# Performance work log

Hardware: AMD Instinct MI355X
Metric: run time of the kernel (lower is better)

The kernel has to match this reference:

```python
import jax, jax.numpy as jnp
import numpy as np

N_C, N_F = 25000, 100000   # coarse / fine node counts
E_C, E_F = 100000, 400000  # coarse / fine edge counts
W, F_IN, F_OUT = 128, 128, 4


def _fnn2(x, w1, b1, w2, b2):
    # 2-layer FNN (fnns_depth=2) with SELU, dropout=0 (eval)
    return jax.nn.selu(x @ w1 + b1) @ w2 + b2


def _interaction(v, e, src, dst, n, ew1, eb1, ew2, eb2, nw1, nb1, nw2, nb2):
    # InteractionNetwork: edge update (gather) -> mean scatter -> node update, residuals
    e = _fnn2(jnp.concatenate([e, v[src], v[dst]], axis=-1), ew1, eb1, ew2, eb2) + e
    s = jax.ops.segment_sum(e, dst, num_segments=n)
    cnt = jax.ops.segment_sum(jnp.ones((e.shape[0], 1), e.dtype), dst, num_segments=n)
    agg = s / jnp.maximum(cnt, 1.0)  # 'mean' aggregation
    v = _fnn2(jnp.concatenate([v, agg], axis=-1), nw1, nb1, nw2, nb2) + v
    return v, e


def setup_inputs() -> dict:
    key = jax.random.key(0)
    ks = iter(jax.random.split(key, 64))
    def rn(shape, scale=1.0):
        return jax.random.normal(next(ks), shape, jnp.float32) * scale
    s3, s2, s1 = 1.0 / np.sqrt(3 * W), 1.0 / np.sqrt(2 * W), 1.0 / np.sqrt(W)
    d = {
        'v': rn((N_C, F_IN)),
        'c_coarse': rn((N_C, W)), 'c_fine': rn((N_F, W)),
        'e_coarse': rn((E_C, W)), 'e_fine': rn((E_F, W)),
        'rel_dist': rn((N_F, 1)),
        'ei_coarse': jax.random.randint(next(ks), (2, E_C), 0, N_C),
        'ei_fine': jax.random.randint(next(ks), (2, E_F), 0, N_F),
        'cluster': jax.random.randint(next(ks), (N_F,), 0, N_C),
        'in_node_w': rn((F_IN, W), 1.0 / np.sqrt(F_IN)), 'in_node_b': rn((W,), 0.01),
        'cond_w': rn((2, W, W), s1), 'cond_b': rn((2, W), 0.01),
        'edge_in_w': rn((2, W, W), s1), 'edge_in_b': rn((2, W), 0.01),
        'bn_ew1': rn((2, 3 * W, W), s3), 'bn_eb1': rn((2, W), 0.01),
        'bn_ew2': rn((2, W, W), s1), 'bn_eb2': rn((2, W), 0.01),
        'bn_nw1': rn((2, 2 * W, W), s2), 'bn_nb1': rn((2, W), 0.01),
        'bn_nw2': rn((2, W, W), s1), 'bn_nb2': rn((2, W), 0.01),
        'unp_w1': rn((W + 1, W), 1.0 / np.sqrt(W + 1)), 'unp_b1': rn((W,), 0.01),
        'unp_w2': rn((W, W), s1), 'unp_b2': rn((W,), 0.01),
        'up_ew1': rn((2, 3 * W, W), s3), 'up_eb1': rn((2, W), 0.01),
        'up_ew2': rn((2, W, W), s1), 'up_eb2': rn((2, W), 0.01),
        'up_nw1': rn((2, 2 * W, W), s2), 'up_nb1': rn((2, W), 0.01),
        'up_nw2': rn((2, W, W), s1), 'up_nb2': rn((2, W), 0.01),
        'out_w': rn((W, F_OUT), s1), 'out_b': rn((F_OUT,), 0.01),
    }
    return d


def reference(v, c_coarse, c_fine, e_coarse, e_fine, rel_dist, ei_coarse, ei_fine, cluster,
              in_node_w, in_node_b, cond_w, cond_b, edge_in_w, edge_in_b,
              bn_ew1, bn_eb1, bn_ew2, bn_eb2, bn_nw1, bn_nb1, bn_nw2, bn_nb2,
              unp_w1, unp_b1, unp_w2, unp_b2,
              up_ew1, up_eb1, up_ew2, up_eb2, up_nw1, up_nb1, up_nw2, up_nb2,
              out_w, out_b):
    src_c, dst_c = ei_coarse[0], ei_coarse[1]
    src_f, dst_f = ei_fine[0], ei_fine[1]
    # input projection + coarse-scale conditioning
    v = v @ in_node_w + in_node_b
    v = v + (c_coarse @ cond_w[0] + cond_b[0])
    e = e_coarse @ edge_in_w[0] + edge_in_b[0]
    # bottleneck InteractionNetwork blocks on coarse graph
    for i in range(bn_ew1.shape[0]):
        v, e = _interaction(v, e, src_c, dst_c, N_C,
                            bn_ew1[i], bn_eb1[i], bn_ew2[i], bn_eb2[i],
                            bn_nw1[i], bn_nb1[i], bn_nw2[i], bn_nb2[i])
    # up block: project skip conditioning/edges, unpool coarse->fine via cluster gather + FNN on [v, scalar rel pos]
    c = c_fine @ cond_w[1] + cond_b[1]
    e = e_fine @ edge_in_w[1] + edge_in_b[1]
    v = _fnn2(jnp.concatenate([v[cluster], rel_dist], axis=-1), unp_w1, unp_b1, unp_w2, unp_b2)
    v = v + c
    for i in range(up_ew1.shape[0]):
        v, e = _interaction(v, e, src_f, dst_f, N_F,
                            up_ew1[i], up_eb1[i], up_ew2[i], up_eb2[i],
                            up_nw1[i], up_nb1[i], up_nw2[i], up_nb2[i])
    return v @ out_w + out_b
```

## Files before the change

### kernel.cpp

```cpp
#include <hip/hip_runtime.h>
#include <hip/hip_bf16.h>

typedef __bf16 bf16_t;
typedef __bf16 bf16x8 __attribute__((ext_vector_type(8)));
typedef float f32x4 __attribute__((ext_vector_type(4)));

#define SELU_SCALE 1.0507009873554805f
#define SELU_ALPHA 1.6732632423543772f

__device__ __forceinline__ float selu_f(float x) {
    return x > 0.0f ? SELU_SCALE * x : SELU_SCALE * SELU_ALPHA * (__expf(x) - 1.0f);
}

__device__ __forceinline__ int4 load8(const void* p, size_t elem_off, int isf) {
    if (!isf) return *(const int4*)((const bf16_t*)p + elem_off);
    const float* f = (const float*)p + elem_off;
    float4 a = ((const float4*)f)[0], b = ((const float4*)f)[1];
    union { int4 i; bf16_t h[8]; } u;
    u.h[0] = (bf16_t)a.x; u.h[1] = (bf16_t)a.y; u.h[2] = (bf16_t)a.z; u.h[3] = (bf16_t)a.w;
    u.h[4] = (bf16_t)b.x; u.h[5] = (bf16_t)b.y; u.h[6] = (bf16_t)b.z; u.h[7] = (bf16_t)b.w;
    return u.i;
}

__global__ void detect_dtype(const unsigned short* p, int* flag) {
    if (threadIdx.x == 0) {
        float m = 0.0f;
        for (int i = 0; i < 128; i++) {
            unsigned int u = ((unsigned int)p[i]) << 16;
            float v = __uint_as_float(u);
            v = fabsf(v);
            if (!(v <= 1e3f)) { m = 1e30f; break; }
            m = fmaxf(m, v);
        }
        *flag = (m > 1e3f) ? 1 : 0;
    }
}

struct VDesc { const void* s; bf16_t* d; int eoff; int n; };
struct VArgs { VDesc v[19]; };
__global__ void convert_vecs(VArgs a, const int* __restrict__ flag) {
    int isf = *flag;
    VDesc vd = a.v[blockIdx.y];
    int i = blockIdx.x * 256 + threadIdx.x;
    if (i < vd.n) {
        size_t idx = (size_t)vd.eoff + i;
        vd.d[i] = isf ? (bf16_t)(((const float*)vd.s)[idx]) : ((const bf16_t*)vd.s)[idx];
    }
}

struct TDesc { const void* s; bf16_t* d; int eoff; int Ksrc; int Ktot; int koff; };
struct TArgs { TDesc t[31]; };
__global__ void transpose_all(TArgs a, const int* __restrict__ flag) {
    int isf = *flag;
    TDesc td = a.t[blockIdx.y];
    int i = blockIdx.x * 256 + threadIdx.x;
    if (i < 128 * td.Ksrc) {
        int n = i / td.Ksrc;
        int k = i - n * td.Ksrc;
        size_t si = (size_t)td.eoff + (size_t)k * 128 + n;
        bf16_t v = isf ? (bf16_t)(((const float*)td.s)[si]) : ((const bf16_t*)td.s)[si];
        td.d[(size_t)n * td.Ktot + td.koff + k] = v;
    }
}

__global__ void count_dst(const int* __restrict__ dst, int* __restrict__ cnt, int E) {
    int e = blockIdx.x * 256 + threadIdx.x;
    if (e < E) atomicAdd(&cnt[dst[e]], 1);
}

__global__ void seg_alloc(const int* __restrict__ cnt, int* __restrict__ rp,
                          int* __restrict__ total, int n) {
    int i = blockIdx.x * 256 + threadIdx.x;
    if (i < n) rp[i] = atomicAdd(total, cnt[i]);
}

__global__ void init_cursor(const int* __restrict__ rp, int* __restrict__ cur, int n) {
    int i = blockIdx.x * 256 + threadIdx.x;
    if (i < n) cur[i] = rp[i];
}

__global__ void csr_scatter(const int* __restrict__ dst, int* __restrict__ cur,
                            int* __restrict__ eids, int E) {
    int e = blockIdx.x * 256 + threadIdx.x;
    if (e < E) {
        unsigned s = (unsigned)atomicAdd(&cur[dst[e]], 1);
        if (s < (unsigned)E) eids[s] = e;
    }
}

template<int K, int N>
__global__ __launch_bounds__(256) void lin1(
    int M, const void* __restrict__ A0, const void* __restrict__ A1,
    const bf16_t* __restrict__ Wt, const bf16_t* __restrict__ b1,
    const bf16_t* __restrict__ b2, const bf16_t* __restrict__ res,
    bf16_t* __restrict__ out, const int* __restrict__ flag)
{
    constexpr int SA = K + 8;
    constexpr int NCT = N / 64;
    __shared__ bf16_t sA[64 * SA];
    const int isf = *flag;
    const int tid = threadIdx.x;
    const int row0 = blockIdx.x * 64;
    const int lane16 = tid & 15;
    const int rgrp = tid >> 4;

    #pragma unroll
    for (int chunk = 0; chunk < K; chunk += 128) {
        const void* sp = chunk ? A1 : A0;
        for (int r = rgrp; r < 64; r += 16) {
            int rr = row0 + r; if (rr >= M) rr = M - 1;
            int4 u = load8(sp, (size_t)rr * 128 + lane16 * 8, isf);
            *(int4*)&sA[r * SA + chunk + lane16 * 8] = u;
        }
    }
    __syncthreads();

    const int lane = tid & 63, wave = tid >> 6;
    const int l15 = lane & 15, lk = lane >> 4;
    const int colbase = wave * (N / 4);
    f32x4 acc[4][NCT];
    const f32x4 zero = {0.f, 0.f, 0.f, 0.f};
    for (int rt = 0; rt < 4; rt++)
        for (int ct = 0; ct < NCT; ct++) acc[rt][ct] = zero;

    #pragma unroll
    for (int k0 = 0; k0 < K; k0 += 32) {
        bf16x8 wv[NCT];
        #pragma unroll
        for (int ct = 0; ct < NCT; ct++)
            wv[ct] = *(const bf16x8*)(Wt + (size_t)(colbase + ct * 16 + l15) * K + k0 + lk * 8);
        #pragma unroll
        for (int rt = 0; rt < 4; rt++) {
            bf16x8 av = *(const bf16x8*)(&sA[(rt * 16 + l15) * SA + k0 + lk * 8]);
            #pragma unroll
            for (int ct = 0; ct < NCT; ct++)
                acc[rt][ct] = __builtin_amdgcn_mfma_f32_16x16x32_bf16(av, wv[ct], acc[rt][ct], 0, 0, 0);
        }
    }

    #pragma unroll
    for (int rt = 0; rt < 4; rt++)
        #pragma unroll
        for (int ct = 0; ct < NCT; ct++) {
            int col = colbase + ct * 16 + l15;
            float bc = (float)b1[col] + (b2 ? (float)b2[col] : 0.0f);
            #pragma unroll
            for (int r = 0; r < 4; r++) {
                int grow = row0 + rt * 16 + lk * 4 + r;
                if (grow < M) {
                    float x = acc[rt][ct][r] + bc;
                    if (res) x += (float)res[(size_t)grow * N + col];
                    out[(size_t)grow * N + col] = (bf16_t)x;
                }
            }
        }
}

template<int MODE>
__global__ __launch_bounds__(512, 8) void fnn2k(
    int M,
    const bf16_t* __restrict__ A0, const bf16_t* __restrict__ Psd,
    const int* __restrict__ g0, const int* __restrict__ g1,
    const bf16_t* __restrict__ Emat, const int* __restrict__ rp,
    const int* __restrict__ degc, const int* __restrict__ eids,
    const bf16_t* __restrict__ W1t, const bf16_t* __restrict__ b1,
    const bf16_t* __restrict__ W2t, const bf16_t* __restrict__ b2,
    const bf16_t* __restrict__ relb, const bf16_t* __restrict__ w1last,
    const bf16_t* __restrict__ res, bf16_t* __restrict__ out,
    const bf16_t* __restrict__ finw, const bf16_t* __restrict__ finb,
    void* __restrict__ fout, const int* __restrict__ flag)
{
    constexpr int NP = (MODE == 3) ? 1 : 2;
    constexpr int K1 = (MODE == 2) ? 256 : 128;
    constexpr int PL = 64 * 136;
    __shared__ bf16_t sA[NP * PL];
    bf16_t* sH = sA + (NP - 1) * PL;

    const int isf = *flag;
    const int tid = threadIdx.x;
    const int lane16 = tid & 15;
    const int rgrp = tid >> 4;
    const int lane = tid & 63, wave = tid >> 6;
    const int l15 = lane & 15, lk = lane >> 4;
    const int colbase = wave * 16;
    const int row0 = blockIdx.x * 64;
    const bool res_lds = (res == A0);
    const f32x4 zero = {0.f, 0.f, 0.f, 0.f};

    #pragma unroll
    for (int c = 0; c < NP; c++) {
        #pragma unroll
        for (int i = 0; i < 2; i++) {
            int r = rgrp + i * 32;
            int rr = row0 + r; if (rr >= M) rr = M - 1;
            int4 u;
            if (MODE == 1 && c == 1) {
                bf16x8 pa = *(const bf16x8*)(Psd + (size_t)g0[rr] * 256 + lane16 * 8);
                bf16x8 pb = *(const bf16x8*)(Psd + (size_t)g1[rr] * 256 + 128 + lane16 * 8);
                union { int4 i4; bf16_t h[8]; } w;
                #pragma unroll
                for (int j = 0; j < 8; j++) w.h[j] = (bf16_t)((float)pa[j] + (float)pb[j]);
                u = w.i4;
            } else if (MODE == 2 && c == 1) {
                int beg = rp[rr], deg = degc[rr];
                float a8[8] = {0.f, 0.f, 0.f, 0.f, 0.f, 0.f, 0.f, 0.f};
                for (int e = 0; e < deg; e++) {
                    int eid = eids[beg + e];
                    bf16x8 ev = *(const bf16x8*)(Emat + (size_t)eid * 128 + lane16 * 8);
                    #pragma unroll
                    for (int j = 0; j < 8; j++) a8[j] += (float)ev[j];
                }
                float inv = 1.0f / (float)(deg > 0 ? deg : 1);
                union { int4 i4; bf16_t h[8]; } w;
                #pragma unroll
                for (int j = 0; j < 8; j++) w.h[j] = (bf16_t)(a8[j] * inv);
                u = w.i4;
            } else {
                const bf16_t* sp = (MODE == 3) ? A0 + (size_t)g0[rr] * 128
                                               : A0 + (size_t)rr * 128;
                u = *(const int4*)(sp + lane16 * 8);
            }
            *(int4*)&sA[c * PL + r * 136 + lane16 * 8] = u;
        }
    }
    __syncthreads();

    f32x4 acc[4];
    #pragma unroll
    for (int rt = 0; rt < 4; rt++) acc[rt] = zero;
    #pragma unroll
    for (int k0 = 0; k0 < K1; k0 += 32) {
        bf16x8 w0 = *(const bf16x8*)(W1t + (size_t)(colbase + l15) * K1 + k0 + lk * 8);
        #pragma unroll
        for (int rt = 0; rt < 4; rt++) {
            bf16x8 av = *(const bf16x8*)(&sA[(k0 / 128) * PL + (rt * 16 + l15) * 136 + (k0 & 127) + lk * 8]);
            acc[rt] = __builtin_amdgcn_mfma_f32_16x16x32_bf16(av, w0, acc[rt], 0, 0, 0);
        }
    }
    if (MODE != 1) __syncthreads();

    {
        int col = colbase + l15;
        float b1c = (float)b1[col];
        float wlc = (MODE == 3) ? (float)w1last[col] : 0.0f;
        #pragma unroll
        for (int rt = 0; rt < 4; rt++)
            #pragma unroll
            for (int r = 0; r < 4; r++) {
                int lrow = rt * 16 + lk * 4 + r;
                int grow = row0 + lrow;
                float x = acc[rt][r] + b1c;
                if (MODE == 1) x += (float)sH[lrow * 136 + col];
                if (MODE == 3) {
                    float rv = (grow < M) ? (float)relb[grow] : 0.0f;
                    x += rv * wlc;
                }
                x = selu_f(x);
                sH[lrow * 136 + col] = (bf16_t)x;
            }
    }
    __syncthreads();

    f32x4 acc2[4];
    #pragma unroll
    for (int rt = 0; rt < 4; rt++) acc2[rt] = zero;
    #pragma unroll
    for (int k0 = 0; k0 < 128; k0 += 32) {
        bf16x8 w0 = *(const bf16x8*)(W2t + (size_t)(colbase + l15) * 128 + k0 + lk * 8);
        #pragma unroll
        for (int rt = 0; rt < 4; rt++) {
            bf16x8 av = *(const bf16x8*)(&sH[(rt * 16 + l15) * 136 + k0 + lk * 8]);
            acc2[rt] = __builtin_amdgcn_mfma_f32_16x16x32_bf16(av, w0, acc2[rt], 0, 0, 0);
        }
    }
    if (finw) __syncthreads();

    {
        int col = colbase + l15;
        float b2c = (float)b2[col];
        #pragma unroll
        for (int rt = 0; rt < 4; rt++)
            #pragma unroll
            for (int r = 0; r < 4; r++) {
                int lrow = rt * 16 + lk * 4 + r;
                int grow = row0 + lrow;
                if (grow < M) {
                    float x = acc2[rt][r] + b2c;
                    if (res) {
                        float rv = (res_lds && NP > 1) ? (float)sA[lrow * 136 + col]
                                                       : (float)res[(size_t)grow * 128 + col];
                        x += rv;
                    }
                    bf16_t xb = (bf16_t)x;
                    if (out) out[(size_t)grow * 128 + col] = xb;
                    if (finw) sH[lrow * 136 + col] = xb;
                }
            }
    }

    if (finw) {
        __syncthreads();
        if (tid < 256) {
            int orow = tid >> 2, c = tid & 3;
            int grow = row0 + orow;
            if (grow < M) {
                float s = (float)finb[c];
                #pragma unroll
                for (int k = 0; k < 128; k++)
                    s += (float)sH[orow * 136 + k] * (float)finw[k * 4 + c];
                if (isf) ((float*)fout)[(size_t)grow * 4 + c] = s;
                else     ((bf16_t*)fout)[(size_t)grow * 4 + c] = (bf16_t)s;
            }
        }
    }
}

extern "C" void kernel_launch(void* const* d_in, const int* in_sizes, int n_in,
                              void* d_out, int out_size, void* d_ws, size_t ws_size,
                              hipStream_t stream) {
    const int NC = 25000, NF = 100000, EC = 100000, EF = 400000;

    const void* v_in      = d_in[0];
    const void* c_coarse  = d_in[1];
    const void* c_fine    = d_in[2];
    const void* e_coarse  = d_in[3];
    const void* e_fine    = d_in[4];
    const void* rel_dist  = d_in[5];
    const int*  ei_c      = (const int*)d_in[6];
    const int*  ei_f      = (const int*)d_in[7];
    const int*  cluster   = (const int*)d_in[8];
    const void* in_node_w = d_in[9];
    const void* in_node_b = d_in[10];
    const void* cond_w    = d_in[11];
    const void* cond_b    = d_in[12];
    const void* edge_in_w = d_in[13];
    const void* edge_in_b = d_in[14];
    const void* bn_ew1    = d_in[15];
    const void* bn_eb1    = d_in[16];
    const void* bn_ew2    = d_in[17];
    const void* bn_eb2    = d_in[18];
    const void* bn_nw1    = d_in[19];
    const void* bn_nb1    = d_in[20];
    const void* bn_nw2    = d_in[21];
    const void* bn_nb2    = d_in[22];
    const void* unp_w1    = d_in[23];
    const void* unp_b1    = d_in[24];
    const void* unp_w2    = d_in[25];
    const void* unp_b2    = d_in[26];
    const void* up_ew1    = d_in[27];
    const void* up_eb1    = d_in[28];
    const void* up_ew2    = d_in[29];
    const void* up_eb2    = d_in[30];
    const void* up_nw1    = d_in[31];
    const void* up_nb1    = d_in[32];
    const void* up_nw2    = d_in[33];
    const void* up_nb2    = d_in[34];
    const void* out_w     = d_in[35];
    const void* out_b     = d_in[36];

    const int* src_c = ei_c, * dst_c = ei_c + EC;
    const int* src_f = ei_f, * dst_f = ei_f + EF;

    char* base = (char*)d_ws;
    size_t off = 0;
    auto carve = [&](size_t bytes) -> void* {
        void* p = base + off;
        off += (bytes + 255) & ~(size_t)255;
        return p;
    };
    int*    flag   = (int*)carve(256);
    int*    zflag  = (int*)carve(256);
    int*    totals = (int*)carve(256);
    bf16_t* vc     = (bf16_t*)carve((size_t)NC * 128 * 2);
    bf16_t* vf     = (bf16_t*)carve((size_t)NF * 128 * 2);
    bf16_t* ef     = (bf16_t*)carve((size_t)EF * 128 * 2);
    bf16_t* ec     = ef;
    bf16_t* Psd    = (bf16_t*)carve((size_t)NF * 256 * 2);
    int*    cnti_c = (int*)carve((size_t)NC * 4);
    int*    cnti_f = (int*)carve((size_t)NF * 4);
    int*    rp_c   = (int*)carve((size_t)NC * 4);
    int*    rp_f   = (int*)carve((size_t)NF * 4);
    int*    cur_c  = (int*)carve((size_t)NC * 4);
    int*    cur_f  = (int*)carve((size_t)NF * 4);

    auto cw = [&](size_t elems) -> bf16_t* { return (bf16_t*)carve(elems * 2); };
    bf16_t* Wic    = cw(128 * 256);
    bf16_t* Wein0  = cw(128 * 128);
    bf16_t* Wein1  = cw(128 * 128);
    bf16_t* Wcond1 = cw(128 * 128);
    bf16_t* Wbe1[2] = { cw(128 * 128), cw(128 * 128) };
    bf16_t* Wsd_c[2] = { cw(256 * 128), cw(256 * 128) };
    bf16_t* Wbe2[2] = { cw(128 * 128), cw(128 * 128) };
    bf16_t* Wbn1[2] = { cw(128 * 256), cw(128 * 256) };
    bf16_t* Wbn2[2] = { cw(128 * 128), cw(128 * 128) };
    bf16_t* Wunp1 = cw(128 * 128);
    bf16_t* Wunp2 = cw(128 * 128);
    bf16_t* Wue1[2] = { cw(128 * 128), cw(128 * 128) };
    bf16_t* Wsd_f[2] = { cw(256 * 128), cw(256 * 128) };
    bf16_t* Wue2[2] = { cw(128 * 128), cw(128 * 128) };
    bf16_t* Wun1[2] = { cw(128 * 256), cw(128 * 256) };
    bf16_t* Wun2[2] = { cw(128 * 128), cw(128 * 128) };
    bf16_t* b_in   = cw(128);
    bf16_t* b_cond = cw(256);
    bf16_t* b_ein  = cw(256);
    bf16_t* b_be1  = cw(256);
    bf16_t* b_be2  = cw(256);
    bf16_t* b_bn1  = cw(256);
    bf16_t* b_bn2  = cw(256);
    bf16_t* b_unp1 = cw(128);
    bf16_t* b_unp2 = cw(128);
    bf16_t* b_ue1  = cw(256);
    bf16_t* b_ue2  = cw(256);
    bf16_t* b_un1  = cw(256);
    bf16_t* b_un2  = cw(256);
    bf16_t* b_out  = cw(8);
    bf16_t* w1last = cw(128);
    bf16_t* relb   = cw(NF);
    bf16_t* foutw  = cw(512);
    bf16_t* zerob  = cw(256);
    int*    eids_c = (int*)carve((size_t)EC * 4);
    int*    eids_f = (int*)carve((size_t)EF * 4);

    detect_dtype<<<1, 64, 0, stream>>>((const unsigned short*)in_node_b, flag);
    hipMemsetAsync(zflag, 0, 256, stream);
    hipMemsetAsync(zerob, 0, 512, stream);

    VArgs va; int vi = 0;
    auto addV = [&](const void* s, bf16_t* d, int eoff, int n) {
        va.v[vi].s = s; va.v[vi].d = d; va.v[vi].eoff = eoff; va.v[vi].n = n; vi++;
    };
    addV(in_node_b, b_in, 0, 128);
    addV(cond_b, b_cond, 0, 256);
    addV(edge_in_b, b_ein, 0, 256);
    addV(bn_eb1, b_be1, 0, 256);  addV(bn_eb2, b_be2, 0, 256);
    addV(bn_nb1, b_bn1, 0, 256);  addV(bn_nb2, b_bn2, 0, 256);
    addV(unp_b1, b_unp1, 0, 128); addV(unp_b2, b_unp2, 0, 128);
    addV(up_eb1, b_ue1, 0, 256);  addV(up_eb2, b_ue2, 0, 256);
    addV(up_nb1, b_un1, 0, 256);  addV(up_nb2, b_un2, 0, 256);
    addV(out_b, b_out, 0, 4);
    addV(unp_w1, w1last, 128 * 128, 128);
    addV(rel_dist, relb, 0, NF);
    addV(out_w, foutw, 0, 512);
    dim3 vg((NF + 255) / 256, vi);
    convert_vecs<<<vg, 256, 0, stream>>>(va, flag);

    TArgs ta; int ti = 0;
    auto addT = [&](const void* s, bf16_t* d, int eoff, int Ksrc, int Ktot, int koff) {
        ta.t[ti].s = s; ta.t[ti].d = d; ta.t[ti].eoff = eoff;
        ta.t[ti].Ksrc = Ksrc; ta.t[ti].Ktot = Ktot; ta.t[ti].koff = koff; ti++;
    };
    addT(in_node_w, Wic, 0, 128, 256, 0);
    addT(cond_w,    Wic, 0, 128, 256, 128);
    addT(edge_in_w, Wein0, 0, 128, 128, 0);
    addT(edge_in_w, Wein1, 16384, 128, 128, 0);
    addT(cond_w,    Wcond1, 16384, 128, 128, 0);
    for (int i = 0; i < 2; i++) {
        addT(bn_ew1, Wbe1[i],           i * 49152,         128, 128, 0);
        addT(bn_ew1, Wsd_c[i],          i * 49152 + 16384, 128, 128, 0);
        addT(bn_ew1, Wsd_c[i] + 16384,  i * 49152 + 32768, 128, 128, 0);
        addT(bn_ew2, Wbe2[i], i * 16384, 128, 128, 0);
        addT(bn_nw1, Wbn1[i], i * 32768, 256, 256, 0);
        addT(bn_nw2, Wbn2[i], i * 16384, 128, 128, 0);
        addT(up_ew1, Wue1[i],           i * 49152,         128, 128, 0);
        addT(up_ew1, Wsd_f[i],          i * 49152 + 16384, 128, 128, 0);
        addT(up_ew1, Wsd_f[i] + 16384,  i * 49152 + 32768, 128, 128, 0);
        addT(up_ew2, Wue2[i], i * 16384, 128, 128, 0);
        addT(up_nw1, Wun1[i], i * 32768, 256, 256, 0);
        addT(up_nw2, Wun2[i], i * 16384, 128, 128, 0);
    }
    addT(unp_w1, Wunp1, 0, 128, 128, 0);
    addT(unp_w2, Wunp2, 0, 128, 128, 0);
    dim3 tg((128 * 256 + 255) / 256, ti);
    transpose_all<<<tg, 256, 0, stream>>>(ta, flag);

    hipMemsetAsync(cnti_c, 0, (size_t)NC * 4, stream);
    hipMemsetAsync(cnti_f, 0, (size_t)NF * 4, stream);
    hipMemsetAsync(totals, 0, 256, stream);
    count_dst<<<(EC + 255) / 256, 256, 0, stream>>>(dst_c, cnti_c, EC);
    count_dst<<<(EF + 255) / 256, 256, 0, stream>>>(dst_f, cnti_f, EF);
    seg_alloc<<<(NC + 255) / 256, 256, 0, stream>>>(cnti_c, rp_c, totals + 0, NC);
    seg_alloc<<<(NF + 255) / 256, 256, 0, stream>>>(cnti_f, rp_f, totals + 1, NF);
    init_cursor<<<(NC + 255) / 256, 256, 0, stream>>>(rp_c, cur_c, NC);
    init_cursor<<<(NF + 255) / 256, 256, 0, stream>>>(rp_f, cur_f, NF);
    csr_scatter<<<(EC + 255) / 256, 256, 0, stream>>>(dst_c, cur_c, eids_c, EC);
    csr_scatter<<<(EF + 255) / 256, 256, 0, stream>>>(dst_f, cur_f, eids_f, EF);

    lin1<256, 128><<<(NC + 63) / 64, 256, 0, stream>>>(NC, v_in, c_coarse, Wic, b_in, b_cond,
                                                       nullptr, vc, flag);
    lin1<128, 128><<<(EC + 63) / 64, 256, 0, stream>>>(EC, e_coarse, nullptr, Wein0, b_ein,
                                                       nullptr, nullptr, ec, flag);

    for (int i = 0; i < 2; i++) {
        lin1<128, 256><<<(NC + 63) / 64, 256, 0, stream>>>(NC, vc, nullptr, Wsd_c[i], zerob,
                                                           nullptr, nullptr, Psd, zflag);
        fnn2k<1><<<(EC + 63) / 64, 512, 0, stream>>>(
            EC, ec, Psd, src_c, dst_c, nullptr, nullptr, nullptr, nullptr,
            Wbe1[i], b_be1 + i * 128, Wbe2[i], b_be2 + i * 128,
            nullptr, nullptr, ec, ec, nullptr, nullptr, nullptr, flag);
        fnn2k<2><<<(NC + 63) / 64, 512, 0, stream>>>(
            NC, vc, nullptr, nullptr, nullptr, ec, rp_c, cnti_c, eids_c,
            Wbn1[i], b_bn1 + i * 128, Wbn2[i], b_bn2 + i * 128,
            nullptr, nullptr, vc, vc, nullptr, nullptr, nullptr, flag);
    }

    lin1<128, 128><<<(NF + 63) / 64, 256, 0, stream>>>(NF, c_fine, nullptr, Wcond1, b_cond + 128,
                                                       nullptr, nullptr, vf, flag);
    fnn2k<3><<<(NF + 63) / 64, 512, 0, stream>>>(
        NF, vc, nullptr, cluster, nullptr, nullptr, nullptr, nullptr, nullptr,
        Wunp1, b_unp1, Wunp2, b_unp2,
        relb, w1last, vf, vf, nullptr, nullptr, nullptr, flag);
    lin1<128, 128><<<(EF + 63) / 64, 256, 0, stream>>>(EF, e_fine, nullptr, Wein1, b_ein + 128,
                                                       nullptr, nullptr, ef, flag);

    for (int i = 0; i < 2; i++) {
        lin1<128, 256><<<(NF + 63) / 64, 256, 0, stream>>>(NF, vf, nullptr, Wsd_f[i], zerob,
                                                           nullptr, nullptr, Psd, zflag);
        fnn2k<1><<<(EF + 63) / 64, 512, 0, stream>>>(
            EF, ef, Psd, src_f, dst_f, nullptr, nullptr, nullptr, nullptr,
            Wue1[i], b_ue1 + i * 128, Wue2[i], b_ue2 + i * 128,
            nullptr, nullptr, ef, ef, nullptr, nullptr, nullptr, flag);
        int last = (i == 1);
        fnn2k<2><<<(NF + 63) / 64, 512, 0, stream>>>(
            NF, vf, nullptr, nullptr, nullptr, ef, rp_f, cnti_f, eids_f,
            Wun1[i], b_un1 + i * 128, Wun2[i], b_un2 + i * 128,
            nullptr, nullptr, vf, (last ? nullptr : vf),
            (last ? foutw : nullptr), b_out,
            (last ? d_out : nullptr), flag);
    }
}
```

Baseline: 809.3 us.

## Fuse src/dst node projection into preceding node-update kernels and merge CSR build launches

```diff
diff --git a/kernel.cpp b/kernel.cpp
--- a/kernel.cpp
+++ b/kernel.cpp
@@ -63,24 +63,33 @@
     }
 }
 
-__global__ void count_dst(const int* __restrict__ dst, int* __restrict__ cnt, int E) {
+__global__ void count_dst2(const int* __restrict__ d0, int* __restrict__ c0, int E0,
+                           const int* __restrict__ d1, int* __restrict__ c1, int E1) {
+    const int* dst = blockIdx.y ? d1 : d0;
+    int* cnt = blockIdx.y ? c1 : c0;
+    int E = blockIdx.y ? E1 : E0;
     int e = blockIdx.x * 256 + threadIdx.x;
     if (e < E) atomicAdd(&cnt[dst[e]], 1);
 }
 
-__global__ void seg_alloc(const int* __restrict__ cnt, int* __restrict__ rp,
-                          int* __restrict__ total, int n) {
+__global__ void seg_alloc2(const int* __restrict__ c0, int* __restrict__ rp0, int* __restrict__ cu0, int n0,
+                           const int* __restrict__ c1, int* __restrict__ rp1, int* __restrict__ cu1, int n1,
+                           int* __restrict__ totals) {
+    const int* cnt = blockIdx.y ? c1 : c0;
+    int* rp = blockIdx.y ? rp1 : rp0;
+    int* cu = blockIdx.y ? cu1 : cu0;
+    int n = blockIdx.y ? n1 : n0;
+    int* total = totals + blockIdx.y;
     int i = blockIdx.x * 256 + threadIdx.x;
-    if (i < n) rp[i] = atomicAdd(total, cnt[i]);
-}
-
-__global__ void init_cursor(const int* __restrict__ rp, int* __restrict__ cur, int n) {
-    int i = blockIdx.x * 256 + threadIdx.x;
-    if (i < n) cur[i] = rp[i];
-}
-
-__global__ void csr_scatter(const int* __restrict__ dst, int* __restrict__ cur,
-                            int* __restrict__ eids, int E) {
+    if (i < n) { int s = atomicAdd(total, cnt[i]); rp[i] = s; cu[i] = s; }
+}
+
+__global__ void csr_scatter2(const int* __restrict__ d0, int* __restrict__ cu0, int* __restrict__ e0, int E0,
+                             const int* __restrict__ d1, int* __restrict__ cu1, int* __restrict__ e1, int E1) {
+    const int* dst = blockIdx.y ? d1 : d0;
+    int* cur = blockIdx.y ? cu1 : cu0;
+    int* eids = blockIdx.y ? e1 : e0;
+    int E = blockIdx.y ? E1 : E0;
     int e = blockIdx.x * 256 + threadIdx.x;
     if (e < E) {
         unsigned s = (unsigned)atomicAdd(&cur[dst[e]], 1);
@@ -168,7 +177,9 @@
     const bf16_t* __restrict__ relb, const bf16_t* __restrict__ w1last,
     const bf16_t* __restrict__ res, bf16_t* __restrict__ out,
     const bf16_t* __restrict__ finw, const bf16_t* __restrict__ finb,
-    void* __restrict__ fout, const int* __restrict__ flag)
+    void* __restrict__ fout,
+    const bf16_t* __restrict__ psdw, bf16_t* __restrict__ psdout,
+    const int* __restrict__ flag)
 {
     constexpr int NP = (MODE == 3) ? 1 : 2;
     constexpr int K1 = (MODE == 2) ? 256 : 128;
@@ -185,6 +196,7 @@
     const int colbase = wave * 16;
     const int row0 = blockIdx.x * 64;
     const bool res_lds = (res == A0);
+    const bool stash = (finw != nullptr) || (psdw != nullptr);
     const f32x4 zero = {0.f, 0.f, 0.f, 0.f};
 
     #pragma unroll
@@ -273,7 +285,7 @@
             acc2[rt] = __builtin_amdgcn_mfma_f32_16x16x32_bf16(av, w0, acc2[rt], 0, 0, 0);
         }
     }
-    if (finw) __syncthreads();
+    if (stash) __syncthreads();
 
     {
         int col = colbase + l15;
@@ -293,9 +305,37 @@
                     }
                     bf16_t xb = (bf16_t)x;
                     if (out) out[(size_t)grow * 128 + col] = xb;
-                    if (finw) sH[lrow * 136 + col] = xb;
+                    if (stash) sH[lrow * 136 + col] = xb;
                 }
             }
+    }
+
+    if (psdw) {
+        __syncthreads();
+        const int colb2 = wave * 32;
+        #pragma unroll
+        for (int ct = 0; ct < 2; ct++) {
+            int col = colb2 + ct * 16 + l15;
+            f32x4 ap[4];
+            #pragma unroll
+            for (int rt = 0; rt < 4; rt++) ap[rt] = zero;
+            #pragma unroll
+            for (int k0 = 0; k0 < 128; k0 += 32) {
+                bf16x8 wv = *(const bf16x8*)(psdw + (size_t)col * 128 + k0 + lk * 8);
+                #pragma unroll
+                for (int rt = 0; rt < 4; rt++) {
+                    bf16x8 av = *(const bf16x8*)(&sH[(rt * 16 + l15) * 136 + k0 + lk * 8]);
+                    ap[rt] = __builtin_amdgcn_mfma_f32_16x16x32_bf16(av, wv, ap[rt], 0, 0, 0);
+                }
+            }
+            #pragma unroll
+            for (int rt = 0; rt < 4; rt++)
+                #pragma unroll
+                for (int r = 0; r < 4; r++) {
+                    int grow = row0 + rt * 16 + lk * 4 + r;
+                    if (grow < M) psdout[(size_t)grow * 256 + col] = (bf16_t)ap[rt][r];
+                }
+        }
     }
 
     if (finw) {
@@ -476,55 +516,59 @@
     hipMemsetAsync(cnti_c, 0, (size_t)NC * 4, stream);
     hipMemsetAsync(cnti_f, 0, (size_t)NF * 4, stream);
     hipMemsetAsync(totals, 0, 256, stream);
-    count_dst<<<(EC + 255) / 256, 256, 0, stream>>>(dst_c, cnti_c, EC);
-    count_dst<<<(EF + 255) / 256, 256, 0, stream>>>(dst_f, cnti_f, EF);
-    seg_alloc<<<(NC + 255) / 256, 256, 0, stream>>>(cnti_c, rp_c, totals + 0, NC);
-    seg_alloc<<<(NF + 255) / 256, 256, 0, stream>>>(cnti_f, rp_f, totals + 1, NF);
-    init_cursor<<<(NC + 255) / 256, 256, 0, stream>>>(rp_c, cur_c, NC);
-    init_cursor<<<(NF + 255) / 256, 256, 0, stream>>>(rp_f, cur_f, NF);
-    csr_scatter<<<(EC + 255) / 256, 256, 0, stream>>>(dst_c, cur_c, eids_c, EC);
-    csr_scatter<<<(EF + 255) / 256, 256, 0, stream>>>(dst_f, cur_f, eids_f, EF);
+    dim3 ge((EF + 255) / 256, 2), gn((NF + 255) / 256, 2);
+    count_dst2<<<ge, 256, 0, stream>>>(dst_c, cnti_c, EC, dst_f, cnti_f, EF);
+    seg_alloc2<<<gn, 256, 0, stream>>>(cnti_c, rp_c, cur_c, NC, cnti_f, rp_f, cur_f, NF, totals);
+    csr_scatter2<<<ge, 256, 0, stream>>>(dst_c, cur_c, eids_c, EC, dst_f, cur_f, eids_f, EF);
 
     lin1<256, 128><<<(NC + 63) / 64, 256, 0, stream>>>(NC, v_in, c_coarse, Wic, b_in, b_cond,
                                                        nullptr, vc, flag);
     lin1<128, 128><<<(EC + 63) / 64, 256, 0, stream>>>(EC, e_coarse, nullptr, Wein0, b_ein,
                                                        nullptr, nullptr, ec, flag);
-
-    for (int i = 0; i < 2; i++) {
-        lin1<128, 256><<<(NC + 63) / 64, 256, 0, stream>>>(NC, vc, nullptr, Wsd_c[i], zerob,
-                                                           nullptr, nullptr, Psd, zflag);
-        fnn2k<1><<<(EC + 63) / 64, 512, 0, stream>>>(
-            EC, ec, Psd, src_c, dst_c, nullptr, nullptr, nullptr, nullptr,
-            Wbe1[i], b_be1 + i * 128, Wbe2[i], b_be2 + i * 128,
-            nullptr, nullptr, ec, ec, nullptr, nullptr, nullptr, flag);
-        fnn2k<2><<<(NC + 63) / 64, 512, 0, stream>>>(
-            NC, vc, nullptr, nullptr, nullptr, ec, rp_c, cnti_c, eids_c,
-            Wbn1[i], b_bn1 + i * 128, Wbn2[i], b_bn2 + i * 128,
-            nullptr, nullptr, vc, vc, nullptr, nullptr, nullptr, flag);
-    }
+    lin1<128, 256><<<(NC + 63) / 64, 256, 0, stream>>>(NC, vc, nullptr, Wsd_c[0], zerob,
+                                                       nullptr, nullptr, Psd, zflag);
+
+    fnn2k<1><<<(EC + 63) / 64, 512, 0, stream>>>(
+        EC, ec, Psd, src_c, dst_c, nullptr, nullptr, nullptr, nullptr,
+        Wbe1[0], b_be1, Wbe2[0], b_be2,
+        nullptr, nullptr, ec, ec, nullptr, nullptr, nullptr, nullptr, nullptr, flag);
+    fnn2k<2><<<(NC + 63) / 64, 512, 0, stream>>>(
+        NC, vc, nullptr, nullptr, nullptr, ec, rp_c, cnti_c, eids_c,
+        Wbn1[0], b_bn1, Wbn2[0], b_bn2,
+        nullptr, nullptr, vc, vc, nullptr, nullptr, nullptr, Wsd_c[1], Psd, flag);
+    fnn2k<1><<<(EC + 63) / 64, 512, 0, stream>>>(
+        EC, ec, Psd, src_c, dst_c, nullptr, nullptr, nullptr, nullptr,
+        Wbe1[1], b_be1 + 128, Wbe2[1], b_be2 + 128,
+        nullptr, nullptr, ec, ec, nullptr, nullptr, nullptr, nullptr, nullptr, flag);
+    fnn2k<2><<<(NC + 63) / 64, 512, 0, stream>>>(
+        NC, vc, nullptr, nullptr, nullptr, ec, rp_c, cnti_c, eids_c,
+        Wbn1[1], b_bn1 + 128, Wbn2[1], b_bn2 + 128,
+        nullptr, nullptr, vc, vc, nullptr, nullptr, nullptr, nullptr, nullptr, flag);
 
     lin1<128, 128><<<(NF + 63) / 64, 256, 0, stream>>>(NF, c_fine, nullptr, Wcond1, b_cond + 128,
                                                        nullptr, nullptr, vf, flag);
     fnn2k<3><<<(NF + 63) / 64, 512, 0, stream>>>(
         NF, vc, nullptr, cluster, nullptr, nullptr, nullptr, nullptr, nullptr,
         Wunp1, b_unp1, Wunp2, b_unp2,
-        relb, w1last, vf, vf, nullptr, nullptr, nullptr, flag);
+        relb, w1last, vf, vf, nullptr, nullptr, nullptr, Wsd_f[0], Psd, flag);
     lin1<128, 128><<<(EF + 63) / 64, 256, 0, stream>>>(EF, e_fine, nullptr, Wein1, b_ein + 128,
                                                        nullptr, nullptr, ef, flag);
 
-    for (int i = 0; i < 2; i++) {
-        lin1<128, 256><<<(NF + 63) / 64, 256, 0, stream>>>(NF, vf, nullptr, Wsd_f[i], zerob,
-                                                           nullptr, nullptr, Psd, zflag);
-        fnn2k<1><<<(EF + 63) / 64, 512, 0, stream>>>(
-            EF, ef, Psd, src_f, dst_f, nullptr, nullptr, nullptr, nullptr,
-            Wue1[i], b_ue1 + i * 128, Wue2[i], b_ue2 + i * 128,
-            nullptr, nullptr, ef, ef, nullptr, nullptr, nullptr, flag);
-        int last = (i == 1);
-        fnn2k<2><<<(NF + 63) / 64, 512, 0, stream>>>(
-            NF, vf, nullptr, nullptr, nullptr, ef, rp_f, cnti_f, eids_f,
-            Wun1[i], b_un1 + i * 128, Wun2[i], b_un2 + i * 128,
-            nullptr, nullptr, vf, (last ? nullptr : vf),
-            (last ? foutw : nullptr), b_out,
-            (last ? d_out : nullptr), flag);
-    }
-}
+    fnn2k<1><<<(EF + 63) / 64, 512, 0, stream>>>(
+        EF, ef, Psd, src_f, dst_f, nullptr, nullptr, nullptr, nullptr,
+        Wue1[0], b_ue1, Wue2[0], b_ue2,
+        nullptr, nullptr, ef, ef, nullptr, nullptr, nullptr, nullptr, nullptr, flag);
+    fnn2k<2><<<(NF + 63) / 64, 512, 0, stream>>>(
+        NF, vf, nullptr, nullptr, nullptr, ef, rp_f, cnti_f, eids_f,
+        Wun1[0], b_un1, Wun2[0], b_un2,
+        nullptr, nullptr, vf, vf, nullptr, nullptr, nullptr, Wsd_f[1], Psd, flag);
+    fnn2k<1><<<(EF + 63) / 64, 512, 0, stream>>>(
+        EF, ef, Psd, src_f, dst_f, nullptr, nullptr, nullptr, nullptr,
+        Wue1[1], b_ue1 + 128, Wue2[1], b_ue2 + 128,
+        nullptr, nullptr, ef, ef, nullptr, nullptr, nullptr, nullptr, nullptr, flag);
+    fnn2k<2><<<(NF + 63) / 64, 512, 0, stream>>>(
+        NF, vf, nullptr, nullptr, nullptr, ef, rp_f, cnti_f, eids_f,
+        Wun1[1], b_un1 + 128, Wun2[1], b_un2 + 128,
+        nullptr, nullptr, vf, nullptr,
+        foutw, b_out, d_out, nullptr, nullptr, flag);
+}
```

Result: slower. 920.6 us (+13.7%).
